# Kernel optimization log

Measured on AMD Instinct MI355X. Metric: run time of the kernel, lower is better.

The kernel has to match this reference:

```python
import jax, jax.numpy as jnp
import numpy as np

TRAN_DIM = 768
N_HEADS = 8
HEAD_DIM = 96
INNER = N_HEADS * HEAD_DIM  # 768


def setup_inputs() -> dict:
    key = jax.random.key(0)
    k1, k2, k3, k4, k5 = jax.random.split(key, 5)
    x = jax.random.normal(k1, (16, 1024, TRAN_DIM), dtype=jnp.float32)
    s_in = 1.0 / np.sqrt(TRAN_DIM)
    W_qkv = jax.random.uniform(k2, (TRAN_DIM, INNER * 3), jnp.float32, -s_in, s_in)
    b_qkv = jax.random.uniform(k3, (INNER * 3,), jnp.float32, -s_in, s_in)
    s_o = 1.0 / np.sqrt(INNER)
    W_out = jax.random.uniform(k4, (INNER, TRAN_DIM), jnp.float32, -s_o, s_o)
    b_out = jax.random.uniform(k5, (TRAN_DIM,), jnp.float32, -s_o, s_o)
    return {"x": x, "W_qkv": W_qkv, "b_qkv": b_qkv, "W_out": W_out, "b_out": b_out}


def reference(x, W_qkv, b_qkv, W_out, b_out):
    B, N, _ = x.shape
    qkv = x @ W_qkv + b_qkv  # [B, N, 3*INNER]
    q, k, v = jnp.split(qkv, 3, axis=-1)
    # [B, N, INNER] -> [B, H, N, D]
    def to_heads(t):
        return t.reshape(B, N, N_HEADS, HEAD_DIM).transpose(0, 2, 1, 3)
    q, k, v = to_heads(q), to_heads(k), to_heads(v)
    scale = HEAD_DIM ** (-0.5)
    dots = jnp.einsum('bhnd,bhmd->bhnm', q, k) * scale
    attn = jax.nn.softmax(dots, axis=-1)
    out = jnp.einsum('bhnm,bhmd->bhnd', attn, v)
    out = out.transpose(0, 2, 1, 3).reshape(B, N, INNER)
    return out @ W_out + b_out
```

## Files before the change

### kernel.cpp

```cpp
#include <hip/hip_runtime.h>
#include <hip/hip_bf16.h>


#define DEVINL __device__ __forceinline__

typedef __attribute__((ext_vector_type(8))) short s16x8;
typedef __attribute__((ext_vector_type(4))) short s16x4;
typedef __attribute__((ext_vector_type(4))) float f32x4;

DEVINL short f2bf(float f) {
  union { float f; unsigned u; } c; c.f = f;
  unsigned r = c.u + 0x7FFFu + ((c.u >> 16) & 1u);
  return (short)(r >> 16);
}
DEVINL float asf(unsigned u) {
  union { unsigned u; float f; } c; c.u = u; return c.f;
}
DEVINL unsigned pack2(float a, float b) {
  union { float f; unsigned u; } ca, cb; ca.f = a; cb.f = b;
  return (ca.u >> 16) | (cb.u & 0xffff0000u);
}

DEVINL void gload_lds16(const short* g, short* lds) {
  __builtin_amdgcn_global_load_lds((const __attribute__((address_space(1))) void*)g,
                                   (__attribute__((address_space(3))) void*)lds, 16, 0, 0);
}


__global__ void cvt_x_kernel(const float* __restrict__ in, short* __restrict__ out) {
  int i = blockIdx.x * 256 + threadIdx.x;
  float4 v = ((const float4*)in)[i];
  s16x4 o = { f2bf(v.x), f2bf(v.y), f2bf(v.z), f2bf(v.w) };
  *(s16x4*)(out + (size_t)i * 4) = o;
}

__global__ void tcvt_kernel(const float* __restrict__ in, short* __restrict__ out, int R, int C) {
  __shared__ float t[32][33];
  int tx = threadIdx.x & 31, ty = threadIdx.x >> 5;
  int r0 = blockIdx.y * 32, c0 = blockIdx.x * 32;
#pragma unroll
  for (int i = 0; i < 4; i++) {
    int r = ty + i * 8;
    t[r][tx] = in[(size_t)(r0 + r) * C + c0 + tx];
  }
  __syncthreads();
#pragma unroll
  for (int i = 0; i < 4; i++) {
    int r = ty + i * 8;
    out[(size_t)(c0 + r) * R + r0 + tx] = f2bf(t[tx][r]);
  }
}

__global__ void vtrans_kernel(const short* __restrict__ qkvb, short* __restrict__ out) {
  __shared__ short t[32][34];
  int tx = threadIdx.x & 31, ty = threadIdx.x >> 5;
  int d0 = blockIdx.x * 32, n0 = blockIdx.y * 32;
  int pair = blockIdx.z;
  int b = pair >> 3, h = pair & 7;
#pragma unroll
  for (int i = 0; i < 4; i++) {
    int r = ty + i * 8;
    t[r][tx] = qkvb[(size_t)(b * 1024 + n0 + r) * 2304 + 1536 + h * 96 + d0 + tx];
  }
  __syncthreads();
  size_t obase = (size_t)pair * 96 * 1024;
#pragma unroll
  for (int i = 0; i < 4; i++) {
    int r = ty + i * 8;
    out[obase + (size_t)(d0 + r) * 1024 + n0 + tx] = t[tx][r];
  }
}


template <int MODE>
__global__ __launch_bounds__(512, 2) void gemm256(const short* __restrict__ A, const short* __restrict__ Bt,
                                                  const float* __restrict__ bias, int K, int nTn,
                                                  short* __restrict__ qkvb, float* __restrict__ outf) {
  __shared__ short lds[65536];
  short* const ldsA = lds;
  short* const ldsB = lds + 32768;
  const int tid = threadIdx.x;
  const int l = tid & 63, w = tid >> 6;
  const int lo = l & 15, hi = l >> 4;
  const int wm = w >> 2, wn = w & 3;

  int cpx = gridDim.x >> 3;
  int bid = blockIdx.x;
  int swz = (bid & 7) * cpx + (bid >> 3);
  int tm = swz / nTn, tn = swz - tm * nTn;

  const int NKT = K >> 6;
  const int NIT = NKT >> 1;

  const int rS = tid >> 3;
  const int ko = (((tid & 7) ^ (rS & 7)) << 3);
  const short* aS = A + (size_t)(tm * 256 + rS) * K + ko;
  const short* bS = Bt + (size_t)(tn * 256 + ((rS >> 5) << 6) + (rS & 31)) * K + ko;
  const size_t step128 = (size_t)128 * K;

  f32x4 acc[8][4] = {};

#define STAGE_A(kt, q, buf) do {                                        \
    const short* s_ = aS + (size_t)(q) * 64 * K + (kt) * 64;            \
    short* d_ = ldsA + ((buf) * 2 + (q)) * 8192 + tid * 8;              \
    gload_lds16(s_, d_); gload_lds16(s_ + step128, d_ + 4096); } while (0)
#define STAGE_B(kt, q, buf) do {                                        \
    const short* s_ = bS + (size_t)(q) * 32 * K + (kt) * 64;            \
    short* d_ = ldsB + ((buf) * 2 + (q)) * 8192 + tid * 8;              \
    gload_lds16(s_, d_); gload_lds16(s_ + step128, d_ + 4096); } while (0)

#define DS_A(AF, bufc, qm) do {                                                   \
    const short* p_ = ldsA + ((bufc) * 2 + (qm)) * 8192 + (wm * 64 + lo) * 64;    \
    _Pragma("unroll") for (int mi = 0; mi < 4; mi++)                              \
      _Pragma("unroll") for (int kk = 0; kk < 2; kk++)                            \
        AF[mi][kk] = *(const s16x8*)(p_ + mi * 1024 + (((kk * 4 + hi) ^ (lo & 7)) << 3)); } while (0)
#define DS_B(BF, bufc, qn) do {                                                   \
    const short* p_ = ldsB + ((bufc) * 2 + (qn)) * 8192 + (wn * 32 + lo) * 64;    \
    _Pragma("unroll") for (int ni = 0; ni < 2; ni++)                              \
      _Pragma("unroll") for (int kk = 0; kk < 2; kk++)                            \
        BF[ni][kk] = *(const s16x8*)(p_ + ni * 1024 + (((kk * 4 + hi) ^ (lo & 7)) << 3)); } while (0)

#define BAR() do { __builtin_amdgcn_sched_barrier(0); __builtin_amdgcn_s_barrier(); \
                   __builtin_amdgcn_sched_barrier(0); } while (0)
#define MFMA16(qm, qn, AF, BF) do {                                               \
    __builtin_amdgcn_s_setprio(1);                                                \
    _Pragma("unroll") for (int kk = 0; kk < 2; kk++)                              \
      _Pragma("unroll") for (int mi = 0; mi < 4; mi++)                            \
        _Pragma("unroll") for (int ni = 0; ni < 2; ni++)                          \
          acc[(qm) * 4 + mi][(qn) * 2 + ni] = __builtin_amdgcn_mfma_f32_16x16x32_bf16( \
              AF[mi][kk], BF[ni][kk], acc[(qm) * 4 + mi][(qn) * 2 + ni], 0, 0, 0); \
    __builtin_amdgcn_s_setprio(0);                                                \
    __builtin_amdgcn_sched_barrier(0); } while (0)

  STAGE_A(0, 0, 0); STAGE_B(0, 0, 0);
  STAGE_A(0, 1, 0); STAGE_B(0, 1, 0);
  STAGE_A(1, 0, 1); STAGE_B(1, 0, 1);
  asm volatile("s_waitcnt vmcnt(4)" ::: "memory");
  __builtin_amdgcn_s_barrier();

  s16x8 af[4][2], bfa[2][2], bfb[2][2];
#pragma unroll 1
  for (int i = 0; i < NIT; i++) {
    int T = 2 * i;
    bool last = (i == NIT - 1);
    DS_A(af, 0, 0); DS_B(bfa, 0, 0);
    if (T + 1 < NKT) STAGE_A(T + 1, 1, 1);
    BAR(); MFMA16(0, 0, af, bfa); BAR();
    DS_B(bfb, 0, 1);
    if (T + 1 < NKT) STAGE_B(T + 1, 1, 1);
    BAR(); MFMA16(0, 1, af, bfb); BAR();
    DS_A(af, 0, 1);
    if (T + 2 < NKT) STAGE_A(T + 2, 0, 0);
    BAR(); MFMA16(1, 0, af, bfa); BAR();
    if (T + 2 < NKT) STAGE_B(T + 2, 0, 0);
    BAR(); MFMA16(1, 1, af, bfb);
    if (last) { asm volatile("s_waitcnt vmcnt(0)" ::: "memory"); }
    else      { asm volatile("s_waitcnt vmcnt(4)" ::: "memory"); }
    BAR();
    DS_A(af, 1, 0); DS_B(bfa, 1, 0);
    if (T + 2 < NKT) STAGE_A(T + 2, 1, 0);
    BAR(); MFMA16(0, 0, af, bfa); BAR();
    DS_B(bfb, 1, 1);
    if (T + 2 < NKT) STAGE_B(T + 2, 1, 0);
    BAR(); MFMA16(0, 1, af, bfb); BAR();
    DS_A(af, 1, 1);
    if (T + 3 < NKT) STAGE_A(T + 3, 0, 1);
    BAR(); MFMA16(1, 0, af, bfa); BAR();
    if (T + 3 < NKT) STAGE_B(T + 3, 0, 1);
    BAR(); MFMA16(1, 1, af, bfb);
    if (!last) { asm volatile("s_waitcnt vmcnt(4)" ::: "memory"); }
    BAR();
  }
#undef STAGE_A
#undef STAGE_B
#undef DS_A
#undef DS_B
#undef BAR
#undef MFMA16

  if (MODE == 0) {
    const float qscale = 0.10206207261596575f;
#pragma unroll
    for (int ni = 0; ni < 4; ni++) {
      int colr = wn * 64 + ni * 16 + lo;
      int coln = tn * 256 + colr;
      float bv = bias[coln];
      float scl = (coln < 768) ? qscale : 1.0f;
#pragma unroll
      for (int mi = 0; mi < 8; mi++)
#pragma unroll
        for (int j = 0; j < 4; j++) {
          int rowr = wm * 128 + mi * 16 + hi * 4 + j;
          lds[rowr * 256 + colr] = f2bf((acc[mi][ni][j] + bv) * scl);
        }
    }
    __syncthreads();
    short* dstb = qkvb + (size_t)(tm * 256) * 2304 + tn * 256;
#pragma unroll
    for (int k = 0; k < 16; k++) {
      int g = k * 512 + tid;
      int r = g >> 5, c = g & 31;
      *(s16x8*)(dstb + (size_t)r * 2304 + c * 8) = *(const s16x8*)(lds + r * 256 + c * 8);
    }
  } else {
#pragma unroll
    for (int ni = 0; ni < 4; ni++) {
      int coln = tn * 256 + wn * 64 + ni * 16 + lo;
      float bv = bias[coln];
#pragma unroll
      for (int mi = 0; mi < 8; mi++) {
#pragma unroll
        for (int j = 0; j < 4; j++) {
          int rowm = tm * 256 + wm * 128 + mi * 16 + hi * 4 + j;
          outf[(size_t)rowm * 768 + coln] = acc[mi][ni][j] + bv;
        }
      }
    }
  }
}


__global__ __launch_bounds__(256) void attn_kernel(const short* __restrict__ qkvb,
                                                   const short* __restrict__ vtb,
                                                   short* __restrict__ attn_out) {
  __shared__ short Klds[64 * 104];
  __shared__ short Vlds[96 * 64];
  int tid = threadIdx.x, lane = tid & 63, wid = tid >> 6;
  int lo = lane & 15, hi = lane >> 4;
  int bid = blockIdx.x;
  int pair = bid & 127, qt = bid >> 7;
  int b = pair >> 3, h = pair & 7;
  const short* Vtp = vtb + (size_t)pair * 1024 * 96;
  int qrow0 = qt * 128 + wid * 32;

  s16x8 qf[2][3];
#pragma unroll
  for (int mq = 0; mq < 2; mq++)
#pragma unroll
    for (int dk = 0; dk < 3; dk++)
      qf[mq][dk] = *(const s16x8*)(qkvb + (size_t)(b * 1024 + qrow0 + mq * 16 + lo) * 2304 +
                                   h * 96 + dk * 32 + hi * 8);

  const short* kp[3];
  const short* vp[3];
  short* kdst[3];
  short* vdst[3];
#pragma unroll
  for (int i = 0; i < 3; i++) {
    int c = i * 256 + tid;
    int krow = c / 12, kcc = c - krow * 12;
    kdst[i] = Klds + krow * 104 + kcc * 8;
    kp[i] = qkvb + (size_t)(b * 1024 + krow) * 2304 + 768 + h * 96 + kcc * 8;
    int vrow = c >> 3, vcc = c & 7;
    vdst[i] = Vlds + vrow * 64 + ((vcc ^ (vrow & 7)) * 8);
    vp[i] = Vtp + (size_t)vrow * 1024 + vcc * 8;
  }

  f32x4 accO[2][6] = {};
  float lsum[2] = {0.0f, 0.0f};

  s16x8 kreg[3], vreg[3];
#pragma unroll
  for (int i = 0; i < 3; i++) {
    kreg[i] = *(const s16x8*)kp[i];
    vreg[i] = *(const s16x8*)vp[i];
  }

  for (int t = 0; t < 16; t++) {
    __syncthreads();
#pragma unroll
    for (int i = 0; i < 3; i++) {
      *(s16x8*)kdst[i] = kreg[i];
      *(s16x8*)vdst[i] = vreg[i];
    }
    __syncthreads();

    int t2 = (t + 1) & 15;
#pragma unroll
    for (int i = 0; i < 3; i++) {
      kreg[i] = *(const s16x8*)(kp[i] + (size_t)t2 * 64 * 2304);
      vreg[i] = *(const s16x8*)(vp[i] + t2 * 64);
    }

    f32x4 st[4][2] = {};
#pragma unroll
    for (int kb2 = 0; kb2 < 4; kb2++) {
#pragma unroll
      for (int dk = 0; dk < 3; dk++) {
        s16x8 kf = *(const s16x8*)(Klds + (kb2 * 16 + lo) * 104 + dk * 32 + hi * 8);
        st[kb2][0] = __builtin_amdgcn_mfma_f32_16x16x32_bf16(kf, qf[0][dk], st[kb2][0], 0, 0, 0);
        st[kb2][1] = __builtin_amdgcn_mfma_f32_16x16x32_bf16(kf, qf[1][dk], st[kb2][1], 0, 0, 0);
      }
    }

    unsigned u[2][4][2];
#pragma unroll
    for (int mq = 0; mq < 2; mq++)
#pragma unroll
      for (int kb2 = 0; kb2 < 4; kb2++) {
        unsigned w0 = pack2(__expf(st[kb2][mq][0]), __expf(st[kb2][mq][1]));
        unsigned w1 = pack2(__expf(st[kb2][mq][2]), __expf(st[kb2][mq][3]));
        u[mq][kb2][0] = w0;
        u[mq][kb2][1] = w1;
        lsum[mq] += (asf(w0 << 16) + asf(w0 & 0xffff0000u)) +
                    (asf(w1 << 16) + asf(w1 & 0xffff0000u));
      }

    int s0 = ((lane >> 4) & 1) * 32 + lo;
    int s1 = s0 + 16;
    bool hiSel = (lane & 32) != 0;
#pragma unroll
    for (int c2 = 0; c2 < 2; c2++) {
      union { unsigned w[4]; s16x8 v; } pa[2];
#pragma unroll
      for (int mq = 0; mq < 2; mq++) {
        unsigned a0 = (unsigned)__shfl((int)u[mq][2 * c2][0], s0, 64);
        unsigned b0 = (unsigned)__shfl((int)u[mq][2 * c2 + 1][0], s0, 64);
        unsigned a1 = (unsigned)__shfl((int)u[mq][2 * c2][1], s0, 64);
        unsigned b1 = (unsigned)__shfl((int)u[mq][2 * c2 + 1][1], s0, 64);
        unsigned a2 = (unsigned)__shfl((int)u[mq][2 * c2][0], s1, 64);
        unsigned b2 = (unsigned)__shfl((int)u[mq][2 * c2 + 1][0], s1, 64);
        unsigned a3 = (unsigned)__shfl((int)u[mq][2 * c2][1], s1, 64);
        unsigned b3 = (unsigned)__shfl((int)u[mq][2 * c2 + 1][1], s1, 64);
        pa[mq].w[0] = hiSel ? b0 : a0;
        pa[mq].w[1] = hiSel ? b1 : a1;
        pa[mq].w[2] = hiSel ? b2 : a2;
        pa[mq].w[3] = hiSel ? b3 : a3;
      }
#pragma unroll
      for (int db = 0; db < 6; db++) {
        int d = db * 16 + lo;
        s16x8 vf = *(const s16x8*)(Vlds + d * 64 + (((c2 * 4 + hi) ^ (d & 7)) * 8));
        accO[0][db] = __builtin_amdgcn_mfma_f32_16x16x32_bf16(pa[0].v, vf, accO[0][db], 0, 0, 0);
        accO[1][db] = __builtin_amdgcn_mfma_f32_16x16x32_bf16(pa[1].v, vf, accO[1][db], 0, 0, 0);
      }
    }
  }

  float rj[2][4];
#pragma unroll
  for (int mq = 0; mq < 2; mq++) {
    float s = lsum[mq];
    s += __shfl_xor(s, 16, 64);
    s += __shfl_xor(s, 32, 64);
    float r = 1.0f / s;
#pragma unroll
    for (int j = 0; j < 4; j++)
      rj[mq][j] = __shfl(r, hi * 4 + j, 64);
  }

#pragma unroll
  for (int mq = 0; mq < 2; mq++)
#pragma unroll
    for (int db = 0; db < 6; db++)
#pragma unroll
      for (int j = 0; j < 4; j++) {
        int qrow = qrow0 + mq * 16 + hi * 4 + j;
        int d = db * 16 + lo;
        attn_out[((size_t)b * 1024 + qrow) * 768 + h * 96 + d] = f2bf(accO[mq][db][j] * rj[mq][j]);
      }
}


extern "C" void kernel_launch(void* const* d_in, const int* in_sizes, int n_in,
                              void* d_out, int out_size, void* d_ws, size_t ws_size,
                              hipStream_t stream) {
  const float* x = (const float*)d_in[0];
  const float* Wqkv = (const float*)d_in[1];
  const float* bqkv = (const float*)d_in[2];
  const float* Wout = (const float*)d_in[3];
  const float* bout = (const float*)d_in[4];
  float* out = (float*)d_out;

  char* ws = (char*)d_ws;
  short* xb = (short*)ws;
  short* wqkvT = (short*)(ws + 25165824);
  short* woutT = (short*)(ws + 28704768);
  short* qkvb = (short*)(ws + 29884416);
  short* vtb = (short*)(ws + 105381888);

  cvt_x_kernel<<<12288, 256, 0, stream>>>(x, xb);
  tcvt_kernel<<<dim3(72, 24), 256, 0, stream>>>(Wqkv, wqkvT, 768, 2304);
  tcvt_kernel<<<dim3(24, 24), 256, 0, stream>>>(Wout, woutT, 768, 768);

  gemm256<0><<<576, 512, 0, stream>>>(xb, wqkvT, bqkv, 768, 9, qkvb, nullptr);
  vtrans_kernel<<<dim3(3, 32, 128), 256, 0, stream>>>(qkvb, vtb);
  attn_kernel<<<1024, 256, 0, stream>>>(qkvb, vtb, xb);
  gemm256<1><<<192, 512, 0, stream>>>(xb, woutT, bout, 768, 3, nullptr, out);
}
```

Measured before the change: 219.2 us.

## Split attention into 8 waves of 16 query rows and use exp2 with folded scale

The attention kernel now launches 512 threads per block, with each wave handling 16 query rows instead of 32, and K/V tile staging is redistributed over all threads. The log2(e) factor is folded into the Q scale so the softmax can use the hardware exp2 directly instead of __expf. This aims to raise occupancy and latency hiding and to trim exponent arithmetic, at the cost of less register-level reuse of each K/V LDS fragment, so LDS reads per MFMA double.

```diff
diff --git a/kernel.cpp b/kernel.cpp
--- a/kernel.cpp
+++ b/kernel.cpp
@@ -179,7 +179,7 @@
 #undef MFMA16
 
   if (MODE == 0) {
-    const float qscale = 0.10206207261596575f;
+    const float qscale = 0.14724444757204526f;
 #pragma unroll
     for (int ni = 0; ni < 4; ni++) {
       int colr = wn * 64 + ni * 16 + lo;
@@ -220,7 +220,7 @@
 }
 
 
-__global__ __launch_bounds__(256) void attn_kernel(const short* __restrict__ qkvb,
+__global__ __launch_bounds__(512) void attn_kernel(const short* __restrict__ qkvb,
                                                    const short* __restrict__ vtb,
                                                    short* __restrict__ attn_out) {
   __shared__ short Klds[64 * 104];
@@ -231,134 +231,123 @@
   int pair = bid & 127, qt = bid >> 7;
   int b = pair >> 3, h = pair & 7;
   const short* Vtp = vtb + (size_t)pair * 1024 * 96;
-  int qrow0 = qt * 128 + wid * 32;
-
-  s16x8 qf[2][3];
-#pragma unroll
-  for (int mq = 0; mq < 2; mq++)
-#pragma unroll
-    for (int dk = 0; dk < 3; dk++)
-      qf[mq][dk] = *(const s16x8*)(qkvb + (size_t)(b * 1024 + qrow0 + mq * 16 + lo) * 2304 +
-                                   h * 96 + dk * 32 + hi * 8);
-
-  const short* kp[3];
-  const short* vp[3];
-  short* kdst[3];
-  short* vdst[3];
+  int qrow0 = qt * 128 + wid * 16;
+
+  s16x8 qf[3];
+#pragma unroll
+  for (int dk = 0; dk < 3; dk++)
+    qf[dk] = *(const s16x8*)(qkvb + (size_t)(b * 1024 + qrow0 + lo) * 2304 +
+                             h * 96 + dk * 32 + hi * 8);
+
+  const short* sp[3];
+  short* sdst[3];
+  size_t sstep[3];
 #pragma unroll
   for (int i = 0; i < 3; i++) {
-    int c = i * 256 + tid;
-    int krow = c / 12, kcc = c - krow * 12;
-    kdst[i] = Klds + krow * 104 + kcc * 8;
-    kp[i] = qkvb + (size_t)(b * 1024 + krow) * 2304 + 768 + h * 96 + kcc * 8;
-    int vrow = c >> 3, vcc = c & 7;
-    vdst[i] = Vlds + vrow * 64 + ((vcc ^ (vrow & 7)) * 8);
-    vp[i] = Vtp + (size_t)vrow * 1024 + vcc * 8;
-  }
-
-  f32x4 accO[2][6] = {};
-  float lsum[2] = {0.0f, 0.0f};
-
-  s16x8 kreg[3], vreg[3];
-#pragma unroll
-  for (int i = 0; i < 3; i++) {
-    kreg[i] = *(const s16x8*)kp[i];
-    vreg[i] = *(const s16x8*)vp[i];
-  }
+    int c = i * 512 + tid;
+    if (c < 768) {
+      int krow = c / 12, kcc = c - krow * 12;
+      sdst[i] = Klds + krow * 104 + kcc * 8;
+      sp[i] = qkvb + (size_t)(b * 1024 + krow) * 2304 + 768 + h * 96 + kcc * 8;
+      sstep[i] = (size_t)64 * 2304;
+    } else {
+      int d = c - 768;
+      int vrow = d >> 3, vcc = d & 7;
+      sdst[i] = Vlds + vrow * 64 + ((vcc ^ (vrow & 7)) * 8);
+      sp[i] = Vtp + (size_t)vrow * 1024 + vcc * 8;
+      sstep[i] = 64;
+    }
+  }
+
+  f32x4 accO[6] = {};
+  float lsum = 0.0f;
+
+  s16x8 sreg[3];
+#pragma unroll
+  for (int i = 0; i < 3; i++) sreg[i] = *(const s16x8*)sp[i];
 
   for (int t = 0; t < 16; t++) {
     __syncthreads();
 #pragma unroll
-    for (int i = 0; i < 3; i++) {
-      *(s16x8*)kdst[i] = kreg[i];
-      *(s16x8*)vdst[i] = vreg[i];
-    }
+    for (int i = 0; i < 3; i++) *(s16x8*)sdst[i] = sreg[i];
     __syncthreads();
 
     int t2 = (t + 1) & 15;
 #pragma unroll
-    for (int i = 0; i < 3; i++) {
-      kreg[i] = *(const s16x8*)(kp[i] + (size_t)t2 * 64 * 2304);
-      vreg[i] = *(const s16x8*)(vp[i] + t2 * 64);
-    }
-
-    f32x4 st[4][2] = {};
+    for (int i = 0; i < 3; i++)
+      sreg[i] = *(const s16x8*)(sp[i] + (size_t)t2 * sstep[i]);
+
+    f32x4 st[4] = {};
 #pragma unroll
     for (int kb2 = 0; kb2 < 4; kb2++) {
 #pragma unroll
       for (int dk = 0; dk < 3; dk++) {
         s16x8 kf = *(const s16x8*)(Klds + (kb2 * 16 + lo) * 104 + dk * 32 + hi * 8);
-        st[kb2][0] = __builtin_amdgcn_mfma_f32_16x16x32_bf16(kf, qf[0][dk], st[kb2][0], 0, 0, 0);
-        st[kb2][1] = __builtin_amdgcn_mfma_f32_16x16x32_bf16(kf, qf[1][dk], st[kb2][1], 0, 0, 0);
+        st[kb2] = __builtin_amdgcn_mfma_f32_16x16x32_bf16(kf, qf[dk], st[kb2], 0, 0, 0);
       }
     }
 
-    unsigned u[2][4][2];
-#pragma unroll
-    for (int mq = 0; mq < 2; mq++)
-#pragma unroll
-      for (int kb2 = 0; kb2 < 4; kb2++) {
-        unsigned w0 = pack2(__expf(st[kb2][mq][0]), __expf(st[kb2][mq][1]));
-        unsigned w1 = pack2(__expf(st[kb2][mq][2]), __expf(st[kb2][mq][3]));
-        u[mq][kb2][0] = w0;
-        u[mq][kb2][1] = w1;
-        lsum[mq] += (asf(w0 << 16) + asf(w0 & 0xffff0000u)) +
-                    (asf(w1 << 16) + asf(w1 & 0xffff0000u));
-      }
+    unsigned u[4][2];
+#pragma unroll
+    for (int kb2 = 0; kb2 < 4; kb2++) {
+      float p0 = __builtin_amdgcn_exp2f(st[kb2][0]);
+      float p1 = __builtin_amdgcn_exp2f(st[kb2][1]);
+      float p2 = __builtin_amdgcn_exp2f(st[kb2][2]);
+      float p3 = __builtin_amdgcn_exp2f(st[kb2][3]);
+      unsigned w0 = pack2(p0, p1);
+      unsigned w1 = pack2(p2, p3);
+      u[kb2][0] = w0;
+      u[kb2][1] = w1;
+      lsum += (asf(w0 << 16) + asf(w0 & 0xffff0000u)) +
+              (asf(w1 << 16) + asf(w1 & 0xffff0000u));
+    }
 
     int s0 = ((lane >> 4) & 1) * 32 + lo;
     int s1 = s0 + 16;
     bool hiSel = (lane & 32) != 0;
 #pragma unroll
     for (int c2 = 0; c2 < 2; c2++) {
-      union { unsigned w[4]; s16x8 v; } pa[2];
-#pragma unroll
-      for (int mq = 0; mq < 2; mq++) {
-        unsigned a0 = (unsigned)__shfl((int)u[mq][2 * c2][0], s0, 64);
-        unsigned b0 = (unsigned)__shfl((int)u[mq][2 * c2 + 1][0], s0, 64);
-        unsigned a1 = (unsigned)__shfl((int)u[mq][2 * c2][1], s0, 64);
-        unsigned b1 = (unsigned)__shfl((int)u[mq][2 * c2 + 1][1], s0, 64);
-        unsigned a2 = (unsigned)__shfl((int)u[mq][2 * c2][0], s1, 64);
-        unsigned b2 = (unsigned)__shfl((int)u[mq][2 * c2 + 1][0], s1, 64);
-        unsigned a3 = (unsigned)__shfl((int)u[mq][2 * c2][1], s1, 64);
-        unsigned b3 = (unsigned)__shfl((int)u[mq][2 * c2 + 1][1], s1, 64);
-        pa[mq].w[0] = hiSel ? b0 : a0;
-        pa[mq].w[1] = hiSel ? b1 : a1;
-        pa[mq].w[2] = hiSel ? b2 : a2;
-        pa[mq].w[3] = hiSel ? b3 : a3;
+      union { unsigned w[4]; s16x8 v; } pa;
+      {
+        unsigned a0 = (unsigned)__shfl((int)u[2 * c2][0], s0, 64);
+        unsigned b0 = (unsigned)__shfl((int)u[2 * c2 + 1][0], s0, 64);
+        unsigned a1 = (unsigned)__shfl((int)u[2 * c2][1], s0, 64);
+        unsigned b1 = (unsigned)__shfl((int)u[2 * c2 + 1][1], s0, 64);
+        unsigned a2 = (unsigned)__shfl((int)u[2 * c2][0], s1, 64);
+        unsigned b2 = (unsigned)__shfl((int)u[2 * c2 + 1][0], s1, 64);
+        unsigned a3 = (unsigned)__shfl((int)u[2 * c2][1], s1, 64);
+        unsigned b3 = (unsigned)__shfl((int)u[2 * c2 + 1][1], s1, 64);
+        pa.w[0] = hiSel ? b0 : a0;
+        pa.w[1] = hiSel ? b1 : a1;
+        pa.w[2] = hiSel ? b2 : a2;
+        pa.w[3] = hiSel ? b3 : a3;
       }
 #pragma unroll
       for (int db = 0; db < 6; db++) {
         int d = db * 16 + lo;
         s16x8 vf = *(const s16x8*)(Vlds + d * 64 + (((c2 * 4 + hi) ^ (d & 7)) * 8));
-        accO[0][db] = __builtin_amdgcn_mfma_f32_16x16x32_bf16(pa[0].v, vf, accO[0][db], 0, 0, 0);
-        accO[1][db] = __builtin_amdgcn_mfma_f32_16x16x32_bf16(pa[1].v, vf, accO[1][db], 0, 0, 0);
+        accO[db] = __builtin_amdgcn_mfma_f32_16x16x32_bf16(pa.v, vf, accO[db], 0, 0, 0);
       }
     }
   }
 
-  float rj[2][4];
-#pragma unroll
-  for (int mq = 0; mq < 2; mq++) {
-    float s = lsum[mq];
-    s += __shfl_xor(s, 16, 64);
-    s += __shfl_xor(s, 32, 64);
-    float r = 1.0f / s;
-#pragma unroll
-    for (int j = 0; j < 4; j++)
-      rj[mq][j] = __shfl(r, hi * 4 + j, 64);
-  }
-
-#pragma unroll
-  for (int mq = 0; mq < 2; mq++)
-#pragma unroll
-    for (int db = 0; db < 6; db++)
-#pragma unroll
-      for (int j = 0; j < 4; j++) {
-        int qrow = qrow0 + mq * 16 + hi * 4 + j;
-        int d = db * 16 + lo;
-        attn_out[((size_t)b * 1024 + qrow) * 768 + h * 96 + d] = f2bf(accO[mq][db][j] * rj[mq][j]);
-      }
+  float s = lsum;
+  s += __shfl_xor(s, 16, 64);
+  s += __shfl_xor(s, 32, 64);
+  float r = 1.0f / s;
+  float rj[4];
+#pragma unroll
+  for (int j = 0; j < 4; j++)
+    rj[j] = __shfl(r, hi * 4 + j, 64);
+
+#pragma unroll
+  for (int db = 0; db < 6; db++)
+#pragma unroll
+    for (int j = 0; j < 4; j++) {
+      int qrow = qrow0 + hi * 4 + j;
+      int d = db * 16 + lo;
+      attn_out[((size_t)b * 1024 + qrow) * 768 + h * 96 + d] = f2bf(accO[db][j] * rj[j]);
+    }
 }
 
 
@@ -385,6 +374,6 @@
 
   gemm256<0><<<576, 512, 0, stream>>>(xb, wqkvT, bqkv, 768, 9, qkvb, nullptr);
   vtrans_kernel<<<dim3(3, 32, 128), 256, 0, stream>>>(qkvb, vtb);
-  attn_kernel<<<1024, 256, 0, stream>>>(qkvb, vtb, xb);
+  attn_kernel<<<1024, 512, 0, stream>>>(qkvb, vtb, xb);
   gemm256<1><<<192, 512, 0, stream>>>(xb, woutT, bout, 768, 3, nullptr, out);
 }
```

Result: no change. 222.2 us (+1.4%).
